# Performance work log

Hardware: AMD Instinct MI355X
Metric: run time of the kernel (lower is better)

## Reference

```python
import jax, jax.numpy as jnp
import numpy as np

B, N, C, H, NH, NC = 4, 2048, 256, 128, 8, 3  # batch, points, in_ch, hidden, heads, classes
DH = H // NH


def setup_inputs() -> dict:
    key = jax.random.key(0)
    ki = iter(jax.random.split(key, 48))
    def w(shape, s=0.05):
        return jax.random.normal(next(ki), shape, jnp.float32) * s
    z = lambda n: jnp.zeros((n,), jnp.float32)
    o = lambda n: jnp.ones((n,), jnp.float32)
    inp = dict(x=jax.random.normal(next(ki), (B, N, C), jnp.float32))
    inp.update(fuse_w1=w((H, C)), fuse_b1=z(H), fuse_w2=w((H, H)), fuse_b2=z(H))
    for l in range(2):
        inp[f'attn{l}_in_w'] = w((3 * H, H)); inp[f'attn{l}_in_b'] = z(3 * H)
        inp[f'attn{l}_out_w'] = w((H, H)); inp[f'attn{l}_out_b'] = z(H)
        inp[f'ffn{l}_w1'] = w((2 * H, H)); inp[f'ffn{l}_b1'] = z(2 * H)
        inp[f'ffn{l}_w2'] = w((H, 2 * H)); inp[f'ffn{l}_b2'] = z(H)
        inp[f'ln{2*l}_g'] = o(H); inp[f'ln{2*l}_b'] = z(H)
        inp[f'ln{2*l+1}_g'] = o(H); inp[f'ln{2*l+1}_b'] = z(H)
    inp.update(out_w1=w((H, H)), out_b1=z(H), out_w2=w((NC, H)), out_b2=z(NC))
    inp.update(det_w1=w((H // 2, H)), det_b1=z(H // 2), det_w2=w((1, H // 2)), det_b2=z(1))
    return inp


def _ln(x, g, b):
    m = jnp.mean(x, axis=-1, keepdims=True)
    v = jnp.mean((x - m) ** 2, axis=-1, keepdims=True)
    return (x - m) * jax.lax.rsqrt(v + 1e-5) * g + b


def _mha(x, in_w, in_b, out_w, out_b):
    # nn.MultiheadAttention (batch_first, self-attn), eval mode (no dropout)
    Bq, Nq, _ = x.shape
    qkv = x @ in_w.T + in_b                          # [B,N,3H]
    q, k, v = jnp.split(qkv, 3, axis=-1)
    q = q.reshape(Bq, Nq, NH, DH)
    k = k.reshape(Bq, Nq, NH, DH)
    v = v.reshape(Bq, Nq, NH, DH)
    s = jnp.einsum('bqhd,bkhd->bhqk', q, k) / jnp.sqrt(jnp.float32(DH))
    a = jax.nn.softmax(s, axis=-1)
    o = jnp.einsum('bhqk,bkhd->bqhd', a, v).reshape(Bq, Nq, H)
    return o @ out_w.T + out_b


def _forward(x, fuse_w1, fuse_b1, fuse_w2, fuse_b2,
             attn0_in_w, attn0_in_b, attn0_out_w, attn0_out_b,
             ffn0_w1, ffn0_b1, ffn0_w2, ffn0_b2, ln0_g, ln0_b, ln1_g, ln1_b,
             attn1_in_w, attn1_in_b, attn1_out_w, attn1_out_b,
             ffn1_w1, ffn1_b1, ffn1_w2, ffn1_b2, ln2_g, ln2_b, ln3_g, ln3_b,
             out_w1, out_b1, out_w2, out_b2, det_w1, det_b1, det_w2, det_b2):
    # feature_fusion (dropout = identity in eval)
    h = jnp.maximum(x @ fuse_w1.T + fuse_b1, 0) @ fuse_w2.T + fuse_b2
    layers = [
        (attn0_in_w, attn0_in_b, attn0_out_w, attn0_out_b, ffn0_w1, ffn0_b1, ffn0_w2, ffn0_b2, ln0_g, ln0_b, ln1_g, ln1_b),
        (attn1_in_w, attn1_in_b, attn1_out_w, attn1_out_b, ffn1_w1, ffn1_b1, ffn1_w2, ffn1_b2, ln2_g, ln2_b, ln3_g, ln3_b),
    ]
    for (iw, ib, ow, ob, f1w, f1b, f2w, f2b, g1, be1, g2, be2) in layers:
        h = _ln(h + _mha(h, iw, ib, ow, ob), g1, be1)
        h = _ln(h + (jnp.maximum(h @ f1w.T + f1b, 0) @ f2w.T + f2b), g2, be2)
    refined_logits = jnp.maximum(h @ out_w1.T + out_b1, 0) @ out_w2.T + out_b2   # [B,N,NC]
    head_prob = jax.nn.sigmoid(jnp.maximum(h @ det_w1.T + det_b1, 0) @ det_w2.T + det_b2)[..., 0]  # [B,N]
    quality = jnp.mean(head_prob, axis=1)                                        # [B]
    return refined_logits, head_prob, quality


def reference(x, fuse_w1, fuse_b1, fuse_w2, fuse_b2,
              attn0_in_w, attn0_in_b, attn0_out_w, attn0_out_b,
              ffn0_w1, ffn0_b1, ffn0_w2, ffn0_b2, ln0_g, ln0_b, ln1_g, ln1_b,
              attn1_in_w, attn1_in_b, attn1_out_w, attn1_out_b,
              ffn1_w1, ffn1_b1, ffn1_w2, ffn1_b2, ln2_g, ln2_b, ln3_g, ln3_b,
              out_w1, out_b1, out_w2, out_b2, det_w1, det_b1, det_w2, det_b2):
    return _forward(x, fuse_w1, fuse_b1, fuse_w2, fuse_b2,
                    attn0_in_w, attn0_in_b, attn0_out_w, attn0_out_b,
                    ffn0_w1, ffn0_b1, ffn0_w2, ffn0_b2, ln0_g, ln0_b, ln1_g, ln1_b,
                    attn1_in_w, attn1_in_b, attn1_out_w, attn1_out_b,
                    ffn1_w1, ffn1_b1, ffn1_w2, ffn1_b2, ln2_g, ln2_b, ln3_g, ln3_b,
                    out_w1, out_b1, out_w2, out_b2, det_w1, det_b1, det_w2, det_b2)
```

## Files before the change

kernel.cpp:

```cpp
#include <hip/hip_runtime.h>
#include <cstddef>

constexpr int Bb  = 4;
constexpr int Nn  = 2048;
constexpr int Cc  = 256;
constexpr int Hh  = 128;
constexpr int NHh = 8;
constexpr int DHh = 16;
constexpr int MTOK = Bb * Nn;
#define LOG2E 1.4426950408889634f

typedef __attribute__((ext_vector_type(8))) short bf16x8;
typedef __attribute__((ext_vector_type(4))) short bf16x4;
typedef __attribute__((ext_vector_type(4))) float f32x4;

__device__ __forceinline__ short f32_to_bf16_rne(float f) {
    union { float f; unsigned int u; } c; c.f = f;
    unsigned int r = c.u + 0x7fffu + ((c.u >> 16) & 1u);
    return (short)(r >> 16);
}
__device__ __forceinline__ float bf16_to_f32(short s) {
    union { float f; unsigned int u; } c; c.u = ((unsigned int)(unsigned short)s) << 16;
    return c.f;
}
__device__ __forceinline__ unsigned pack2_bf16(float a, float b) {
    unsigned ua = __float_as_uint(a);
    unsigned ub = __float_as_uint(b);
    ua += 0x7fffu + ((ua >> 16) & 1u);
    ub += 0x7fffu + ((ub >> 16) & 1u);
    return __builtin_amdgcn_perm(ub, ua, 0x07060302);
}

struct CvtJobs {
    const float* src[13];
    short*       dst[13];
    int          off[14];
    float*       qzero;
};

__global__ __launch_bounds__(256) void cvt_kernel(CvtJobs j) {
    const int gid = blockIdx.x * 256 + threadIdx.x;
    if (blockIdx.x == 0 && threadIdx.x < 4) j.qzero[threadIdx.x] = 0.f;
    if (gid >= j.off[13]) return;
    int k = 0;
    #pragma unroll
    for (int i = 0; i < 12; ++i) if (gid >= j.off[i + 1]) k = i + 1;
    const int idx = (gid - j.off[k]) * 4;
    float4 v = *(const float4*)(j.src[k] + idx);
    short o4[4] = { f32_to_bf16_rne(v.x), f32_to_bf16_rne(v.y),
                    f32_to_bf16_rne(v.z), f32_to_bf16_rne(v.w) };
    *(bf16x4*)(j.dst[k] + idx) = *(bf16x4*)o4;
}

__global__ __launch_bounds__(256) void gemm_qkv_kernel(
    const short* __restrict__ X, const short* __restrict__ W,
    const float* __restrict__ bias, short* __restrict__ Yb)
{
    constexpr int K = 128, N = 384;
    __shared__ short As[64 * 40];
    __shared__ short Bs[64 * 40];

    const int tid  = threadIdx.x;
    const int lane = tid & 63;
    const int wv   = tid >> 6;
    const int col  = lane & 15;
    const int g    = lane >> 4;
    const int m0   = blockIdx.y * 64;
    const int n0   = blockIdx.x * 64;
    const int sr   = tid >> 2;
    const int sc   = (tid & 3) * 8;

    f32x4 acc[4] = {};

    for (int k0 = 0; k0 < K; k0 += 32) {
        __syncthreads();
        *(bf16x8*)&As[sr * 40 + sc] =
            *(const bf16x8*)(X + (size_t)(m0 + sr) * K + k0 + sc);
        *(bf16x8*)&Bs[sr * 40 + sc] =
            *(const bf16x8*)(W + (size_t)(n0 + sr) * K + k0 + sc);
        __syncthreads();

        bf16x8 a = *(bf16x8*)&As[(wv * 16 + col) * 40 + g * 8];
        #pragma unroll
        for (int jj = 0; jj < 4; ++jj) {
            bf16x8 b = *(bf16x8*)&Bs[(jj * 16 + col) * 40 + g * 8];
            acc[jj] = __builtin_amdgcn_mfma_f32_16x16x32_bf16(a, b, acc[jj], 0, 0, 0);
        }
    }

    #pragma unroll
    for (int jj = 0; jj < 4; ++jj) {
        const int cn  = n0 + jj * 16 + col;
        const int sec = cn >> 7;
        const int hd  = (cn & 127) >> 4;
        const int d   = cn & 15;
        const float bb = bias[cn];
        #pragma unroll
        for (int r = 0; r < 4; ++r) {
            const int rm = m0 + wv * 16 + g * 4 + r;
            const int bq = rm >> 11, tt = rm & 2047;
            float v = acc[jj][r] + bb;
            Yb[(size_t)sec * (MTOK * 128)
               + ((size_t)(bq * NHh + hd) * Nn + tt) * DHh + d] = f32_to_bf16_rne(v);
        }
    }
}

template<int K, int CR, bool DO_LN>
__global__ __launch_bounds__(256) void gemmln_kernel(
    const short* __restrict__ X, const short* __restrict__ W,
    const float* __restrict__ bias,
    float* __restrict__ hf, short* __restrict__ hb,
    const float* __restrict__ gw, const float* __restrict__ bw)
{
    constexpr int ST  = K + 8;
    constexpr int NCH = 128 / CR;
    constexpr int NF  = CR / 32;
    __shared__ short As[32 * ST];
    __shared__ short Ws[CR * ST];
    __shared__ float P[32 * 130];

    const int tid  = threadIdx.x;
    const int lane = tid & 63;
    const int wv   = tid >> 6;
    const int col  = lane & 15;
    const int g    = lane >> 4;
    const int m0   = blockIdx.x * 32;
    const int mst  = (wv & 1) * 16;
    const int cb   = (wv >> 1) * (CR / 2);

    for (int i = tid; i < 32 * (K / 8); i += 256) {
        const int r = i / (K / 8), c = (i % (K / 8)) * 8;
        *(bf16x8*)&As[r * ST + c] = *(const bf16x8*)(X + (size_t)(m0 + r) * K + c);
    }

    f32x4 ya[NCH][NF] = {};
    #pragma unroll
    for (int ch = 0; ch < NCH; ++ch) {
        for (int i = tid; i < CR * (K / 8); i += 256) {
            const int r = i / (K / 8), c = (i % (K / 8)) * 8;
            *(bf16x8*)&Ws[r * ST + c] =
                *(const bf16x8*)(W + (size_t)(ch * CR + r) * K + c);
        }
        __syncthreads();
        #pragma unroll
        for (int k0 = 0; k0 < K; k0 += 32) {
            bf16x8 a = *(bf16x8*)&As[(mst + col) * ST + k0 + g * 8];
            #pragma unroll
            for (int f = 0; f < NF; ++f) {
                bf16x8 b = *(bf16x8*)&Ws[(cb + f * 16 + col) * ST + k0 + g * 8];
                ya[ch][f] = __builtin_amdgcn_mfma_f32_16x16x32_bf16(a, b, ya[ch][f], 0, 0, 0);
            }
        }
        __syncthreads();
    }

    #pragma unroll
    for (int ch = 0; ch < NCH; ++ch)
        #pragma unroll
        for (int f = 0; f < NF; ++f) {
            const int cn = ch * CR + cb + f * 16 + col;
            const float bb = bias[cn];
            #pragma unroll
            for (int r = 0; r < 4; ++r)
                P[(mst + g * 4 + r) * 130 + cn] = ya[ch][f][r] + bb;
        }
    __syncthreads();

    #pragma unroll
    for (int rr = 0; rr < 8; ++rr) {
        const int row = wv * 8 + rr;
        const size_t t = m0 + row;
        float2 pv = *(float2*)&P[row * 130 + 2 * lane];
        if (DO_LN) {
            float2 hv = ((const float2*)(hf + t * Hh))[lane];
            float a0 = hv.x + pv.x, a1 = hv.y + pv.y;
            float sum = a0 + a1;
            #pragma unroll
            for (int off = 32; off > 0; off >>= 1) sum += __shfl_xor(sum, off);
            const float mean = sum * (1.f / 128.f);
            const float d0 = a0 - mean, d1 = a1 - mean;
            float vs = d0 * d0 + d1 * d1;
            #pragma unroll
            for (int off = 32; off > 0; off >>= 1) vs += __shfl_xor(vs, off);
            const float rstd = rsqrtf(vs * (1.f / 128.f) + 1e-5f);
            float2 gv = ((const float2*)gw)[lane];
            float2 bv = ((const float2*)bw)[lane];
            float2 r = { d0 * rstd * gv.x + bv.x, d1 * rstd * gv.y + bv.y };
            ((float2*)(hf + t * Hh))[lane] = r;
            *(unsigned*)&hb[t * Hh + lane * 2] = pack2_bf16(r.x, r.y);
        } else {
            ((float2*)(hf + t * Hh))[lane] = pv;
            *(unsigned*)&hb[t * Hh + lane * 2] = pack2_bf16(pv.x, pv.y);
        }
    }
}

template<int K, int MID, int CR1, int CR2, bool DO_LN>
__global__ __launch_bounds__(256) void mlp2_kernel(
    const short* __restrict__ X,
    const short* __restrict__ W1, const float* __restrict__ b1,
    const short* __restrict__ W2, const float* __restrict__ b2,
    float* __restrict__ hf, short* __restrict__ hb,
    const float* __restrict__ gw, const float* __restrict__ bw)
{
    constexpr int STA = K + 8;
    constexpr int STU = MID + 8;
    constexpr int WS1 = CR1 * STA;
    constexpr int WS2 = CR2 * STU;
    constexpr int WSZ = (WS1 > WS2) ? WS1 : WS2;
    __shared__ short As[32 * STA];
    __shared__ short Ws[WSZ];
    __shared__ short U[32 * STU];
    __shared__ float P[32 * 130];

    const int tid  = threadIdx.x;
    const int lane = tid & 63;
    const int wv   = tid >> 6;
    const int col  = lane & 15;
    const int g    = lane >> 4;
    const int m0   = blockIdx.x * 32;
    const int mst  = (wv & 1) * 16;

    for (int i = tid; i < 32 * (K / 8); i += 256) {
        const int r = i / (K / 8), c = (i % (K / 8)) * 8;
        *(bf16x8*)&As[r * STA + c] = *(const bf16x8*)(X + (size_t)(m0 + r) * K + c);
    }

    constexpr int NCH1 = MID / CR1;
    constexpr int NF1  = CR1 / 32;
    const int cb1 = (wv >> 1) * (CR1 / 2);
    #pragma unroll
    for (int ch = 0; ch < NCH1; ++ch) {
        for (int i = tid; i < CR1 * (K / 8); i += 256) {
            const int r = i / (K / 8), c = (i % (K / 8)) * 8;
            *(bf16x8*)&Ws[r * STA + c] =
                *(const bf16x8*)(W1 + (size_t)(ch * CR1 + r) * K + c);
        }
        __syncthreads();
        f32x4 ya[NF1] = {};
        #pragma unroll
        for (int k0 = 0; k0 < K; k0 += 32) {
            bf16x8 a = *(bf16x8*)&As[(mst + col) * STA + k0 + g * 8];
            #pragma unroll
            for (int f = 0; f < NF1; ++f) {
                bf16x8 b = *(bf16x8*)&Ws[(cb1 + f * 16 + col) * STA + k0 + g * 8];
                ya[f] = __builtin_amdgcn_mfma_f32_16x16x32_bf16(a, b, ya[f], 0, 0, 0);
            }
        }
        #pragma unroll
        for (int f = 0; f < NF1; ++f) {
            const int cn = ch * CR1 + cb1 + f * 16 + col;
            const float bb = b1[cn];
            #pragma unroll
            for (int r = 0; r < 4; ++r)
                U[(mst + g * 4 + r) * STU + cn] =
                    f32_to_bf16_rne(fmaxf(ya[f][r] + bb, 0.f));
        }
        __syncthreads();
    }

    constexpr int NCH2 = 128 / CR2;
    constexpr int NF2  = CR2 / 32;
    const int cb2 = (wv >> 1) * (CR2 / 2);
    f32x4 yb[NCH2][NF2] = {};
    #pragma unroll
    for (int ch = 0; ch < NCH2; ++ch) {
        for (int i = tid; i < CR2 * (MID / 8); i += 256) {
            const int r = i / (MID / 8), c = (i % (MID / 8)) * 8;
            *(bf16x8*)&Ws[r * STU + c] =
                *(const bf16x8*)(W2 + (size_t)(ch * CR2 + r) * MID + c);
        }
        __syncthreads();
        #pragma unroll
        for (int k0 = 0; k0 < MID; k0 += 32) {
            bf16x8 a = *(bf16x8*)&U[(mst + col) * STU + k0 + g * 8];
            #pragma unroll
            for (int f = 0; f < NF2; ++f) {
                bf16x8 b = *(bf16x8*)&Ws[(cb2 + f * 16 + col) * STU + k0 + g * 8];
                yb[ch][f] = __builtin_amdgcn_mfma_f32_16x16x32_bf16(a, b, yb[ch][f], 0, 0, 0);
            }
        }
        __syncthreads();
    }

    #pragma unroll
    for (int ch = 0; ch < NCH2; ++ch)
        #pragma unroll
        for (int f = 0; f < NF2; ++f) {
            const int cn = ch * CR2 + cb2 + f * 16 + col;
            const float bb = b2[cn];
            #pragma unroll
            for (int r = 0; r < 4; ++r)
                P[(mst + g * 4 + r) * 130 + cn] = yb[ch][f][r] + bb;
        }
    __syncthreads();

    #pragma unroll
    for (int rr = 0; rr < 8; ++rr) {
        const int row = wv * 8 + rr;
        const size_t t = m0 + row;
        float2 pv = *(float2*)&P[row * 130 + 2 * lane];
        if (DO_LN) {
            float2 hv = ((const float2*)(hf + t * Hh))[lane];
            float a0 = hv.x + pv.x, a1 = hv.y + pv.y;
            float sum = a0 + a1;
            #pragma unroll
            for (int off = 32; off > 0; off >>= 1) sum += __shfl_xor(sum, off);
            const float mean = sum * (1.f / 128.f);
            const float d0 = a0 - mean, d1 = a1 - mean;
            float vs = d0 * d0 + d1 * d1;
            #pragma unroll
            for (int off = 32; off > 0; off >>= 1) vs += __shfl_xor(vs, off);
            const float rstd = rsqrtf(vs * (1.f / 128.f) + 1e-5f);
            float2 gv = ((const float2*)gw)[lane];
            float2 bv = ((const float2*)bw)[lane];
            float2 r = { d0 * rstd * gv.x + bv.x, d1 * rstd * gv.y + bv.y };
            ((float2*)(hf + t * Hh))[lane] = r;
            *(unsigned*)&hb[t * Hh + lane * 2] = pack2_bf16(r.x, r.y);
        } else {
            ((float2*)(hf + t * Hh))[lane] = pv;
            *(unsigned*)&hb[t * Hh + lane * 2] = pack2_bf16(pv.x, pv.y);
        }
    }
}

__global__ __launch_bounds__(256) void head_kernel(
    const short* __restrict__ X,
    const short* __restrict__ W1b, const float* __restrict__ b1,
    const short* __restrict__ DW1b, const float* __restrict__ db1,
    const float* __restrict__ w2, const float* __restrict__ b2,
    const float* __restrict__ dw2, const float* __restrict__ db2,
    float* __restrict__ out)
{
    constexpr int K = 128, ST = K + 8;
    __shared__ short As[32 * ST];
    __shared__ short Ws[64 * ST];
    __shared__ float P[32 * 196];

    const int tid  = threadIdx.x;
    const int lane = tid & 63;
    const int wv   = tid >> 6;
    const int col  = lane & 15;
    const int g    = lane >> 4;
    const int m0   = blockIdx.x * 32;
    const int mst  = (wv & 1) * 16;
    const int cb   = (wv >> 1) * 32;

    for (int i = tid; i < 32 * (K / 8); i += 256) {
        const int r = i / (K / 8), c = (i % (K / 8)) * 8;
        *(bf16x8*)&As[r * ST + c] = *(const bf16x8*)(X + (size_t)(m0 + r) * K + c);
    }

    f32x4 ya[3][2] = {};
    #pragma unroll
    for (int ch = 0; ch < 3; ++ch) {
        for (int i = tid; i < 64 * (K / 8); i += 256) {
            const int r = i / (K / 8), c = (i % (K / 8)) * 8;
            const int rg = ch * 64 + r;
            const short* src = (rg < 128) ? (W1b + (size_t)rg * K)
                                          : (DW1b + (size_t)(rg - 128) * K);
            *(bf16x8*)&Ws[r * ST + c] = *(const bf16x8*)(src + c);
        }
        __syncthreads();
        #pragma unroll
        for (int k0 = 0; k0 < K; k0 += 32) {
            bf16x8 a = *(bf16x8*)&As[(mst + col) * ST + k0 + g * 8];
            #pragma unroll
            for (int f = 0; f < 2; ++f) {
                bf16x8 b = *(bf16x8*)&Ws[(cb + f * 16 + col) * ST + k0 + g * 8];
                ya[ch][f] = __builtin_amdgcn_mfma_f32_16x16x32_bf16(a, b, ya[ch][f], 0, 0, 0);
            }
        }
        __syncthreads();
    }

    #pragma unroll
    for (int ch = 0; ch < 3; ++ch)
        #pragma unroll
        for (int f = 0; f < 2; ++f) {
            const int cn = ch * 64 + cb + f * 16 + col;
            const float bb = (cn < 128) ? b1[cn] : db1[cn - 128];
            #pragma unroll
            for (int r = 0; r < 4; ++r)
                P[(mst + g * 4 + r) * 196 + cn] = fmaxf(ya[ch][f][r] + bb, 0.f);
        }
    __syncthreads();

    const float w20 = w2[2 * lane],       w21 = w2[2 * lane + 1];
    const float w22 = w2[128 + 2 * lane], w23 = w2[129 + 2 * lane];
    const float w24 = w2[256 + 2 * lane], w25 = w2[257 + 2 * lane];
    const float dwl = dw2[lane];
    float qacc = 0.f;
    #pragma unroll
    for (int rr = 0; rr < 8; ++rr) {
        const int row = wv * 8 + rr;
        const size_t t = m0 + row;
        const float x0 = P[row * 196 + 2 * lane];
        const float x1 = P[row * 196 + 2 * lane + 1];
        float s0 = x0 * w20 + x1 * w21;
        float s1 = x0 * w22 + x1 * w23;
        float s2 = x0 * w24 + x1 * w25;
        float d  = P[row * 196 + 128 + lane] * dwl;
        #pragma unroll
        for (int off = 32; off > 0; off >>= 1) {
            s0 += __shfl_xor(s0, off);
            s1 += __shfl_xor(s1, off);
            s2 += __shfl_xor(s2, off);
            d  += __shfl_xor(d,  off);
        }
        if (lane == 0) {
            out[t * 3 + 0] = s0 + b2[0];
            out[t * 3 + 1] = s1 + b2[1];
            out[t * 3 + 2] = s2 + b2[2];
            const float prob = 1.f / (1.f + __expf(-(d + db2[0])));
            out[24576 + t] = prob;
            qacc += prob;
        }
    }
    if (lane == 0)
        atomicAdd(&out[32768 + (m0 >> 11)], qacc * (1.f / (float)Nn));
}

constexpr int KT = 128;
constexpr int KS = 28;
constexpr int VS = 132;

__global__ __launch_bounds__(256) void attn_kernel(
    const short* __restrict__ qkv, short* __restrict__ out)
{
    __shared__ short Ks[KT * KS];
    __shared__ short Vs[DHh * VS];

    const int tid  = threadIdx.x;
    const int lane = tid & 63;
    const int wv   = tid >> 6;
    const int col  = lane & 15;
    const int g    = lane >> 4;
    const int hd   = blockIdx.y;
    const int b    = blockIdx.z;
    const int q0   = blockIdx.x * 64 + wv * 16;

    const size_t bh = (size_t)(b * NHh + hd) * Nn * DHh;
    const short* Qh = qkv + bh;
    const short* Kh = qkv + (size_t)MTOK * 128 + bh;
    const short* Vh = qkv + (size_t)2 * MTOK * 128 + bh;

    bf16x8 qf = {};
    if (g < 2) {
        bf16x8 qraw = *(const bf16x8*)(Qh + (size_t)(q0 + col) * DHh + g * 8);
        const float qs = 0.25f * LOG2E;
        #pragma unroll
        for (int i = 0; i < 8; ++i)
            qf[i] = f32_to_bf16_rne(bf16_to_f32(qraw[i]) * qs);
    }

    f32x4 o    = {0.f, 0.f, 0.f, 0.f};
    f32x4 lacc = {0.f, 0.f, 0.f, 0.f};
    const short one_bf16 = (short)0x3F80;
    const bf16x8 ones = { one_bf16, one_bf16, one_bf16, one_bf16,
                          one_bf16, one_bf16, one_bf16, one_bf16 };

    const int ksr = tid >> 1;
    const int ksd = (tid & 1) * 8;
    const int va  = tid >> 2;
    const int vd  = (tid & 3) * 4;

    for (int kt = 0; kt < Nn; kt += KT) {
        __syncthreads();
        {
            *(bf16x8*)&Ks[ksr * KS + ksd] =
                *(const bf16x8*)(Kh + (size_t)(kt + ksr) * DHh + ksd);
            const short* v0 = Vh + (size_t)(kt + 2 * va) * DHh + vd;
            bf16x4 r0 = *(const bf16x4*)v0;
            bf16x4 r1 = *(const bf16x4*)(v0 + DHh);
            unsigned a0 = ((const unsigned*)&r0)[0], a1 = ((const unsigned*)&r0)[1];
            unsigned b0 = ((const unsigned*)&r1)[0], b1 = ((const unsigned*)&r1)[1];
            *(unsigned*)&Vs[(vd + 0) * VS + 2 * va] = __builtin_amdgcn_perm(b0, a0, 0x05040100);
            *(unsigned*)&Vs[(vd + 1) * VS + 2 * va] = __builtin_amdgcn_perm(b0, a0, 0x07060302);
            *(unsigned*)&Vs[(vd + 2) * VS + 2 * va] = __builtin_amdgcn_perm(b1, a1, 0x05040100);
            *(unsigned*)&Vs[(vd + 3) * VS + 2 * va] = __builtin_amdgcn_perm(b1, a1, 0x07060302);
        }
        __syncthreads();

        #pragma unroll
        for (int s = 0; s < 4; ++s) {
            bf16x8 kf0 = {}, kf1 = {};
            if (g < 2) {
                kf0 = *(bf16x8*)&Ks[(s * 32 + col) * KS + g * 8];
                kf1 = *(bf16x8*)&Ks[(s * 32 + 16 + col) * KS + g * 8];
            }
            f32x4 z = {0.f, 0.f, 0.f, 0.f};
            f32x4 sA = __builtin_amdgcn_mfma_f32_16x16x32_bf16(kf0, qf, z, 0, 0, 0);
            f32x4 sB = __builtin_amdgcn_mfma_f32_16x16x32_bf16(kf1, qf, z, 0, 0, 0);

            union { bf16x8 v; unsigned u[4]; } pf;
            pf.u[0] = pack2_bf16(__builtin_amdgcn_exp2f(sA[0]),
                                 __builtin_amdgcn_exp2f(sA[1]));
            pf.u[1] = pack2_bf16(__builtin_amdgcn_exp2f(sA[2]),
                                 __builtin_amdgcn_exp2f(sA[3]));
            pf.u[2] = pack2_bf16(__builtin_amdgcn_exp2f(sB[0]),
                                 __builtin_amdgcn_exp2f(sB[1]));
            pf.u[3] = pack2_bf16(__builtin_amdgcn_exp2f(sB[2]),
                                 __builtin_amdgcn_exp2f(sB[3]));

            bf16x8 vf;
            ((bf16x4*)&vf)[0] = *(bf16x4*)&Vs[col * VS + s * 32 + g * 4];
            ((bf16x4*)&vf)[1] = *(bf16x4*)&Vs[col * VS + s * 32 + 16 + g * 4];

            o    = __builtin_amdgcn_mfma_f32_16x16x32_bf16(pf.v, vf,   o,    0, 0, 0);
            lacc = __builtin_amdgcn_mfma_f32_16x16x32_bf16(pf.v, ones, lacc, 0, 0, 0);
        }
    }

    #pragma unroll
    for (int r = 0; r < 4; ++r) {
        const float inv = __builtin_amdgcn_rcpf(lacc[r]);
        out[(size_t)(b * Nn + q0 + g * 4 + r) * Hh + hd * DHh + col] =
            f32_to_bf16_rne(o[r] * inv);
    }
}

extern "C" void kernel_launch(void* const* d_in, const int* in_sizes, int n_in,
                              void* d_out, int out_size, void* d_ws, size_t ws_size,
                              hipStream_t stream)
{
    char* W8 = (char*)d_ws;
    float* hf   = (float*)(W8 + 0);
    short* hb   = (short*)(W8 + 4194304);
    short* wb   = (short*)(W8 + 6291456);
    char*  regA = W8 + 7340032;
    char*  regB = W8 + 13631488;

    short* xb    = (short*)regA;
    short* qkvb  = (short*)regA;
    short* attno = (short*)regB;
    float* out   = (float*)d_out;

    const int wsz[12]  = {32768,16384,49152,16384,32768,32768,49152,16384,32768,32768,16384,8192};
    const int wsrc[12] = {1, 3, 5, 7, 9, 11, 17, 19, 21, 23, 29, 33};
    int woff[13]; woff[0] = 0;
    for (int i = 0; i < 12; ++i) woff[i + 1] = woff[i] + wsz[i];

    CvtJobs jobs;
    int acc = 0;
    for (int i = 0; i < 12; ++i) {
        jobs.src[i] = (const float*)d_in[wsrc[i]];
        jobs.dst[i] = wb + woff[i];
        jobs.off[i] = acc;
        acc += wsz[i] / 4;
    }
    jobs.src[12] = (const float*)d_in[0];
    jobs.dst[12] = xb;
    jobs.off[12] = acc;
    acc += (MTOK * Cc) / 4;
    jobs.off[13] = acc;
    jobs.qzero = out + 32768;

    hipLaunchKernelGGL(cvt_kernel, dim3((acc + 255) / 256), dim3(256), 0, stream, jobs);

    hipLaunchKernelGGL((mlp2_kernel<256, 128, 32, 64, false>), dim3(MTOK / 32), dim3(256), 0,
                       stream, xb, wb + woff[0], (const float*)d_in[2],
                       wb + woff[1], (const float*)d_in[4], hf, hb, nullptr, nullptr);

    for (int l = 0; l < 2; ++l) {
        const int ib = 5 + l * 12;
        const int wbase = 2 + l * 4;
        hipLaunchKernelGGL(gemm_qkv_kernel, dim3(384 / 64, MTOK / 64), dim3(256), 0, stream,
                           hb, wb + woff[wbase + 0], (const float*)d_in[ib + 1], qkvb);
        hipLaunchKernelGGL(attn_kernel, dim3(Nn / 64, NHh, Bb), dim3(256), 0, stream,
                           qkvb, attno);
        hipLaunchKernelGGL((gemmln_kernel<128, 64, true>), dim3(MTOK / 32), dim3(256), 0, stream,
                           attno, wb + woff[wbase + 1], (const float*)d_in[ib + 3],
                           hf, hb, (const float*)d_in[ib + 8], (const float*)d_in[ib + 9]);
        hipLaunchKernelGGL((mlp2_kernel<128, 256, 64, 32, true>), dim3(MTOK / 32), dim3(256), 0,
                           stream, hb, wb + woff[wbase + 2], (const float*)d_in[ib + 5],
                           wb + woff[wbase + 3], (const float*)d_in[ib + 7],
                           hf, hb, (const float*)d_in[ib + 10], (const float*)d_in[ib + 11]);
    }

    hipLaunchKernelGGL(head_kernel, dim3(MTOK / 32), dim3(256), 0, stream,
                       hb, wb + woff[10], (const float*)d_in[30],
                       wb + woff[11], (const float*)d_in[34],
                       (const float*)d_in[31], (const float*)d_in[32],
                       (const float*)d_in[35], (const float*)d_in[36], out);
}
```

Baseline: 299.9 us.

## Fuse out-proj, LN, FFN and next-layer QKV into per-layer kernels

Result: slower. 306.7 us (+2.3%).

```diff
diff --git a/kernel.cpp b/kernel.cpp
--- a/kernel.cpp
+++ b/kernel.cpp
@@ -52,72 +52,34 @@
     *(bf16x4*)(j.dst[k] + idx) = *(bf16x4*)o4;
 }
 
-__global__ __launch_bounds__(256) void gemm_qkv_kernel(
-    const short* __restrict__ X, const short* __restrict__ W,
-    const float* __restrict__ bias, short* __restrict__ Yb)
+__device__ __forceinline__ void stage_w(short* Ws, const short* src, int rows,
+                                        int kw, int st, int tid) {
+    for (int i = tid; i < rows * (kw / 8); i += 256) {
+        const int r = i / (kw / 8), c = (i % (kw / 8)) * 8;
+        *(bf16x8*)&Ws[r * st + c] = *(const bf16x8*)(src + (size_t)r * kw + c);
+    }
+}
+
+__device__ __forceinline__ void qkv_write(short* qkvb, int rm, int cn, float v) {
+    const int sec = cn >> 7;
+    const int hd  = (cn & 127) >> 4;
+    const int d   = cn & 15;
+    const int bq  = rm >> 11, tt = rm & 2047;
+    qkvb[(size_t)sec * (MTOK * 128)
+         + ((size_t)(bq * NHh + hd) * Nn + tt) * DHh + d] = f32_to_bf16_rne(v);
+}
+
+__global__ __launch_bounds__(256) void fusion_qkv_kernel(
+    const short* __restrict__ X,
+    const short* __restrict__ W1, const float* __restrict__ b1,
+    const short* __restrict__ W2, const float* __restrict__ b2,
+    float* __restrict__ hf, short* __restrict__ hb,
+    const short* __restrict__ Wq, const float* __restrict__ bq,
+    short* __restrict__ qkvb)
 {
-    constexpr int K = 128, N = 384;
-    __shared__ short As[64 * 40];
-    __shared__ short Bs[64 * 40];
-
-    const int tid  = threadIdx.x;
-    const int lane = tid & 63;
-    const int wv   = tid >> 6;
-    const int col  = lane & 15;
-    const int g    = lane >> 4;
-    const int m0   = blockIdx.y * 64;
-    const int n0   = blockIdx.x * 64;
-    const int sr   = tid >> 2;
-    const int sc   = (tid & 3) * 8;
-
-    f32x4 acc[4] = {};
-
-    for (int k0 = 0; k0 < K; k0 += 32) {
-        __syncthreads();
-        *(bf16x8*)&As[sr * 40 + sc] =
-            *(const bf16x8*)(X + (size_t)(m0 + sr) * K + k0 + sc);
-        *(bf16x8*)&Bs[sr * 40 + sc] =
-            *(const bf16x8*)(W + (size_t)(n0 + sr) * K + k0 + sc);
-        __syncthreads();
-
-        bf16x8 a = *(bf16x8*)&As[(wv * 16 + col) * 40 + g * 8];
-        #pragma unroll
-        for (int jj = 0; jj < 4; ++jj) {
-            bf16x8 b = *(bf16x8*)&Bs[(jj * 16 + col) * 40 + g * 8];
-            acc[jj] = __builtin_amdgcn_mfma_f32_16x16x32_bf16(a, b, acc[jj], 0, 0, 0);
-        }
-    }
-
-    #pragma unroll
-    for (int jj = 0; jj < 4; ++jj) {
-        const int cn  = n0 + jj * 16 + col;
-        const int sec = cn >> 7;
-        const int hd  = (cn & 127) >> 4;
-        const int d   = cn & 15;
-        const float bb = bias[cn];
-        #pragma unroll
-        for (int r = 0; r < 4; ++r) {
-            const int rm = m0 + wv * 16 + g * 4 + r;
-            const int bq = rm >> 11, tt = rm & 2047;
-            float v = acc[jj][r] + bb;
-            Yb[(size_t)sec * (MTOK * 128)
-               + ((size_t)(bq * NHh + hd) * Nn + tt) * DHh + d] = f32_to_bf16_rne(v);
-        }
-    }
-}
-
-template<int K, int CR, bool DO_LN>
-__global__ __launch_bounds__(256) void gemmln_kernel(
-    const short* __restrict__ X, const short* __restrict__ W,
-    const float* __restrict__ bias,
-    float* __restrict__ hf, short* __restrict__ hb,
-    const float* __restrict__ gw, const float* __restrict__ bw)
-{
-    constexpr int ST  = K + 8;
-    constexpr int NCH = 128 / CR;
-    constexpr int NF  = CR / 32;
-    __shared__ short As[32 * ST];
-    __shared__ short Ws[CR * ST];
+    __shared__ short As[32 * 264];
+    __shared__ short Ws[8704];
+    __shared__ short U[32 * 136];
     __shared__ float P[32 * 130];
 
     const int tid  = threadIdx.x;
@@ -127,91 +89,121 @@
     const int g    = lane >> 4;
     const int m0   = blockIdx.x * 32;
     const int mst  = (wv & 1) * 16;
-    const int cb   = (wv >> 1) * (CR / 2);
-
-    for (int i = tid; i < 32 * (K / 8); i += 256) {
-        const int r = i / (K / 8), c = (i % (K / 8)) * 8;
-        *(bf16x8*)&As[r * ST + c] = *(const bf16x8*)(X + (size_t)(m0 + r) * K + c);
-    }
-
-    f32x4 ya[NCH][NF] = {};
-    #pragma unroll
-    for (int ch = 0; ch < NCH; ++ch) {
-        for (int i = tid; i < CR * (K / 8); i += 256) {
-            const int r = i / (K / 8), c = (i % (K / 8)) * 8;
-            *(bf16x8*)&Ws[r * ST + c] =
-                *(const bf16x8*)(W + (size_t)(ch * CR + r) * K + c);
-        }
+
+    for (int i = tid; i < 32 * (256 / 8); i += 256) {
+        const int r = i / 32, c = (i % 32) * 8;
+        *(bf16x8*)&As[r * 264 + c] = *(const bf16x8*)(X + (size_t)(m0 + r) * 256 + c);
+    }
+
+    {
+        const int cb1 = (wv >> 1) * 16;
+        #pragma unroll
+        for (int ch = 0; ch < 4; ++ch) {
+            stage_w(Ws, W1 + (size_t)(ch * 32) * 256, 32, 256, 264, tid);
+            __syncthreads();
+            f32x4 ya = {0.f, 0.f, 0.f, 0.f};
+            #pragma unroll
+            for (int k0 = 0; k0 < 256; k0 += 32) {
+                bf16x8 a = *(bf16x8*)&As[(mst + col) * 264 + k0 + g * 8];
+                bf16x8 b = *(bf16x8*)&Ws[(cb1 + col) * 264 + k0 + g * 8];
+                ya = __builtin_amdgcn_mfma_f32_16x16x32_bf16(a, b, ya, 0, 0, 0);
+            }
+            const int cn = ch * 32 + cb1 + col;
+            const float bb = b1[cn];
+            #pragma unroll
+            for (int r = 0; r < 4; ++r)
+                U[(mst + g * 4 + r) * 136 + cn] =
+                    f32_to_bf16_rne(fmaxf(ya[r] + bb, 0.f));
+            __syncthreads();
+        }
+    }
+
+    {
+        const int cb2 = (wv >> 1) * 32;
+        f32x4 yb[2][2] = {};
+        #pragma unroll
+        for (int ch = 0; ch < 2; ++ch) {
+            stage_w(Ws, W2 + (size_t)(ch * 64) * 128, 64, 128, 136, tid);
+            __syncthreads();
+            #pragma unroll
+            for (int k0 = 0; k0 < 128; k0 += 32) {
+                bf16x8 a = *(bf16x8*)&U[(mst + col) * 136 + k0 + g * 8];
+                #pragma unroll
+                for (int f = 0; f < 2; ++f) {
+                    bf16x8 b = *(bf16x8*)&Ws[(cb2 + f * 16 + col) * 136 + k0 + g * 8];
+                    yb[ch][f] = __builtin_amdgcn_mfma_f32_16x16x32_bf16(a, b, yb[ch][f], 0, 0, 0);
+                }
+            }
+            __syncthreads();
+        }
+        #pragma unroll
+        for (int ch = 0; ch < 2; ++ch)
+            #pragma unroll
+            for (int f = 0; f < 2; ++f) {
+                const int cn = ch * 64 + cb2 + f * 16 + col;
+                const float bb = b2[cn];
+                #pragma unroll
+                for (int r = 0; r < 4; ++r)
+                    P[(mst + g * 4 + r) * 130 + cn] = yb[ch][f][r] + bb;
+            }
         __syncthreads();
-        #pragma unroll
-        for (int k0 = 0; k0 < K; k0 += 32) {
-            bf16x8 a = *(bf16x8*)&As[(mst + col) * ST + k0 + g * 8];
-            #pragma unroll
-            for (int f = 0; f < NF; ++f) {
-                bf16x8 b = *(bf16x8*)&Ws[(cb + f * 16 + col) * ST + k0 + g * 8];
-                ya[ch][f] = __builtin_amdgcn_mfma_f32_16x16x32_bf16(a, b, ya[ch][f], 0, 0, 0);
-            }
-        }
-        __syncthreads();
-    }
-
-    #pragma unroll
-    for (int ch = 0; ch < NCH; ++ch)
-        #pragma unroll
-        for (int f = 0; f < NF; ++f) {
-            const int cn = ch * CR + cb + f * 16 + col;
-            const float bb = bias[cn];
-            #pragma unroll
-            for (int r = 0; r < 4; ++r)
-                P[(mst + g * 4 + r) * 130 + cn] = ya[ch][f][r] + bb;
-        }
-    __syncthreads();
+    }
 
     #pragma unroll
     for (int rr = 0; rr < 8; ++rr) {
         const int row = wv * 8 + rr;
         const size_t t = m0 + row;
         float2 pv = *(float2*)&P[row * 130 + 2 * lane];
-        if (DO_LN) {
-            float2 hv = ((const float2*)(hf + t * Hh))[lane];
-            float a0 = hv.x + pv.x, a1 = hv.y + pv.y;
-            float sum = a0 + a1;
-            #pragma unroll
-            for (int off = 32; off > 0; off >>= 1) sum += __shfl_xor(sum, off);
-            const float mean = sum * (1.f / 128.f);
-            const float d0 = a0 - mean, d1 = a1 - mean;
-            float vs = d0 * d0 + d1 * d1;
-            #pragma unroll
-            for (int off = 32; off > 0; off >>= 1) vs += __shfl_xor(vs, off);
-            const float rstd = rsqrtf(vs * (1.f / 128.f) + 1e-5f);
-            float2 gv = ((const float2*)gw)[lane];
-            float2 bv = ((const float2*)bw)[lane];
-            float2 r = { d0 * rstd * gv.x + bv.x, d1 * rstd * gv.y + bv.y };
-            ((float2*)(hf + t * Hh))[lane] = r;
-            *(unsigned*)&hb[t * Hh + lane * 2] = pack2_bf16(r.x, r.y);
-        } else {
-            ((float2*)(hf + t * Hh))[lane] = pv;
-            *(unsigned*)&hb[t * Hh + lane * 2] = pack2_bf16(pv.x, pv.y);
-        }
-    }
-}
-
-template<int K, int MID, int CR1, int CR2, bool DO_LN>
-__global__ __launch_bounds__(256) void mlp2_kernel(
+        ((float2*)(hf + t * Hh))[lane] = pv;
+        const unsigned pk = pack2_bf16(pv.x, pv.y);
+        *(unsigned*)&hb[t * Hh + lane * 2] = pk;
+        *(unsigned*)&U[row * 136 + 2 * lane] = pk;
+    }
+
+    {
+        const int cb = (wv >> 1) * 32;
+        #pragma unroll
+        for (int ch = 0; ch < 6; ++ch) {
+            stage_w(Ws, Wq + (size_t)(ch * 64) * 128, 64, 128, 136, tid);
+            __syncthreads();
+            f32x4 yq[2] = {};
+            #pragma unroll
+            for (int k0 = 0; k0 < 128; k0 += 32) {
+                bf16x8 a = *(bf16x8*)&U[(mst + col) * 136 + k0 + g * 8];
+                #pragma unroll
+                for (int f = 0; f < 2; ++f) {
+                    bf16x8 b = *(bf16x8*)&Ws[(cb + f * 16 + col) * 136 + k0 + g * 8];
+                    yq[f] = __builtin_amdgcn_mfma_f32_16x16x32_bf16(a, b, yq[f], 0, 0, 0);
+                }
+            }
+            #pragma unroll
+            for (int f = 0; f < 2; ++f) {
+                const int cn = ch * 64 + cb + f * 16 + col;
+                const float bb = bq[cn];
+                #pragma unroll
+                for (int r = 0; r < 4; ++r)
+                    qkv_write(qkvb, m0 + mst + g * 4 + r, cn, yq[f][r] + bb);
+            }
+            __syncthreads();
+        }
+    }
+}
+
+template<bool DO_QKV>
+__global__ __launch_bounds__(256) void layer_kernel(
     const short* __restrict__ X,
+    const short* __restrict__ Wo, const float* __restrict__ bo,
+    const float* __restrict__ g1v, const float* __restrict__ be1v,
     const short* __restrict__ W1, const float* __restrict__ b1,
     const short* __restrict__ W2, const float* __restrict__ b2,
+    const float* __restrict__ g2v, const float* __restrict__ be2v,
     float* __restrict__ hf, short* __restrict__ hb,
-    const float* __restrict__ gw, const float* __restrict__ bw)
+    const short* __restrict__ Wq, const float* __restrict__ bq,
+    short* __restrict__ qkvb)
 {
-    constexpr int STA = K + 8;
-    constexpr int STU = MID + 8;
-    constexpr int WS1 = CR1 * STA;
-    constexpr int WS2 = CR2 * STU;
-    constexpr int WSZ = (WS1 > WS2) ? WS1 : WS2;
-    __shared__ short As[32 * STA];
-    __shared__ short Ws[WSZ];
-    __shared__ short U[32 * STU];
+    __shared__ short As[32 * 136];
+    __shared__ short Ws[8704];
+    __shared__ short U[32 * 264];
     __shared__ float P[32 * 130];
 
     const int tid  = threadIdx.x;
@@ -222,105 +214,171 @@
     const int m0   = blockIdx.x * 32;
     const int mst  = (wv & 1) * 16;
 
-    for (int i = tid; i < 32 * (K / 8); i += 256) {
-        const int r = i / (K / 8), c = (i % (K / 8)) * 8;
-        *(bf16x8*)&As[r * STA + c] = *(const bf16x8*)(X + (size_t)(m0 + r) * K + c);
-    }
-
-    constexpr int NCH1 = MID / CR1;
-    constexpr int NF1  = CR1 / 32;
-    const int cb1 = (wv >> 1) * (CR1 / 2);
-    #pragma unroll
-    for (int ch = 0; ch < NCH1; ++ch) {
-        for (int i = tid; i < CR1 * (K / 8); i += 256) {
-            const int r = i / (K / 8), c = (i % (K / 8)) * 8;
-            *(bf16x8*)&Ws[r * STA + c] =
-                *(const bf16x8*)(W1 + (size_t)(ch * CR1 + r) * K + c);
-        }
+    for (int i = tid; i < 32 * (128 / 8); i += 256) {
+        const int r = i / 16, c = (i % 16) * 8;
+        *(bf16x8*)&As[r * 136 + c] = *(const bf16x8*)(X + (size_t)(m0 + r) * 128 + c);
+    }
+
+    {
+        const int cb = (wv >> 1) * 32;
+        f32x4 yo[2][2] = {};
+        #pragma unroll
+        for (int ch = 0; ch < 2; ++ch) {
+            stage_w(Ws, Wo + (size_t)(ch * 64) * 128, 64, 128, 136, tid);
+            __syncthreads();
+            #pragma unroll
+            for (int k0 = 0; k0 < 128; k0 += 32) {
+                bf16x8 a = *(bf16x8*)&As[(mst + col) * 136 + k0 + g * 8];
+                #pragma unroll
+                for (int f = 0; f < 2; ++f) {
+                    bf16x8 b = *(bf16x8*)&Ws[(cb + f * 16 + col) * 136 + k0 + g * 8];
+                    yo[ch][f] = __builtin_amdgcn_mfma_f32_16x16x32_bf16(a, b, yo[ch][f], 0, 0, 0);
+                }
+            }
+            __syncthreads();
+        }
+        #pragma unroll
+        for (int ch = 0; ch < 2; ++ch)
+            #pragma unroll
+            for (int f = 0; f < 2; ++f) {
+                const int cn = ch * 64 + cb + f * 16 + col;
+                const float bb = bo[cn];
+                #pragma unroll
+                for (int r = 0; r < 4; ++r)
+                    P[(mst + g * 4 + r) * 130 + cn] = yo[ch][f][r] + bb;
+            }
         __syncthreads();
-        f32x4 ya[NF1] = {};
-        #pragma unroll
-        for (int k0 = 0; k0 < K; k0 += 32) {
-            bf16x8 a = *(bf16x8*)&As[(mst + col) * STA + k0 + g * 8];
-            #pragma unroll
-            for (int f = 0; f < NF1; ++f) {
-                bf16x8 b = *(bf16x8*)&Ws[(cb1 + f * 16 + col) * STA + k0 + g * 8];
-                ya[f] = __builtin_amdgcn_mfma_f32_16x16x32_bf16(a, b, ya[f], 0, 0, 0);
-            }
-        }
-        #pragma unroll
-        for (int f = 0; f < NF1; ++f) {
-            const int cn = ch * CR1 + cb1 + f * 16 + col;
-            const float bb = b1[cn];
-            #pragma unroll
-            for (int r = 0; r < 4; ++r)
-                U[(mst + g * 4 + r) * STU + cn] =
-                    f32_to_bf16_rne(fmaxf(ya[f][r] + bb, 0.f));
-        }
-        __syncthreads();
-    }
-
-    constexpr int NCH2 = 128 / CR2;
-    constexpr int NF2  = CR2 / 32;
-    const int cb2 = (wv >> 1) * (CR2 / 2);
-    f32x4 yb[NCH2][NF2] = {};
-    #pragma unroll
-    for (int ch = 0; ch < NCH2; ++ch) {
-        for (int i = tid; i < CR2 * (MID / 8); i += 256) {
-            const int r = i / (MID / 8), c = (i % (MID / 8)) * 8;
-            *(bf16x8*)&Ws[r * STU + c] =
-                *(const bf16x8*)(W2 + (size_t)(ch * CR2 + r) * MID + c);
-        }
-        __syncthreads();
-        #pragma unroll
-        for (int k0 = 0; k0 < MID; k0 += 32) {
-            bf16x8 a = *(bf16x8*)&U[(mst + col) * STU + k0 + g * 8];
-            #pragma unroll
-            for (int f = 0; f < NF2; ++f) {
-                bf16x8 b = *(bf16x8*)&Ws[(cb2 + f * 16 + col) * STU + k0 + g * 8];
-                yb[ch][f] = __builtin_amdgcn_mfma_f32_16x16x32_bf16(a, b, yb[ch][f], 0, 0, 0);
-            }
-        }
-        __syncthreads();
-    }
-
-    #pragma unroll
-    for (int ch = 0; ch < NCH2; ++ch)
-        #pragma unroll
-        for (int f = 0; f < NF2; ++f) {
-            const int cn = ch * CR2 + cb2 + f * 16 + col;
-            const float bb = b2[cn];
-            #pragma unroll
-            for (int r = 0; r < 4; ++r)
-                P[(mst + g * 4 + r) * 130 + cn] = yb[ch][f][r] + bb;
-        }
-    __syncthreads();
-
+    }
+
+    float2 res[8];
     #pragma unroll
     for (int rr = 0; rr < 8; ++rr) {
         const int row = wv * 8 + rr;
         const size_t t = m0 + row;
         float2 pv = *(float2*)&P[row * 130 + 2 * lane];
-        if (DO_LN) {
-            float2 hv = ((const float2*)(hf + t * Hh))[lane];
-            float a0 = hv.x + pv.x, a1 = hv.y + pv.y;
-            float sum = a0 + a1;
-            #pragma unroll
-            for (int off = 32; off > 0; off >>= 1) sum += __shfl_xor(sum, off);
-            const float mean = sum * (1.f / 128.f);
-            const float d0 = a0 - mean, d1 = a1 - mean;
-            float vs = d0 * d0 + d1 * d1;
-            #pragma unroll
-            for (int off = 32; off > 0; off >>= 1) vs += __shfl_xor(vs, off);
-            const float rstd = rsqrtf(vs * (1.f / 128.f) + 1e-5f);
-            float2 gv = ((const float2*)gw)[lane];
-            float2 bv = ((const float2*)bw)[lane];
-            float2 r = { d0 * rstd * gv.x + bv.x, d1 * rstd * gv.y + bv.y };
-            ((float2*)(hf + t * Hh))[lane] = r;
-            *(unsigned*)&hb[t * Hh + lane * 2] = pack2_bf16(r.x, r.y);
-        } else {
-            ((float2*)(hf + t * Hh))[lane] = pv;
-            *(unsigned*)&hb[t * Hh + lane * 2] = pack2_bf16(pv.x, pv.y);
+        float2 hv = ((const float2*)(hf + t * Hh))[lane];
+        float a0 = hv.x + pv.x, a1 = hv.y + pv.y;
+        float sum = a0 + a1;
+        #pragma unroll
+        for (int off = 32; off > 0; off >>= 1) sum += __shfl_xor(sum, off);
+        const float mean = sum * (1.f / 128.f);
+        const float d0 = a0 - mean, d1 = a1 - mean;
+        float vs = d0 * d0 + d1 * d1;
+        #pragma unroll
+        for (int off = 32; off > 0; off >>= 1) vs += __shfl_xor(vs, off);
+        const float rstd = rsqrtf(vs * (1.f / 128.f) + 1e-5f);
+        float2 gv = ((const float2*)g1v)[lane];
+        float2 bv = ((const float2*)be1v)[lane];
+        float2 r = { d0 * rstd * gv.x + bv.x, d1 * rstd * gv.y + bv.y };
+        res[rr] = r;
+        *(unsigned*)&As[row * 136 + 2 * lane] = pack2_bf16(r.x, r.y);
+    }
+
+    {
+        const int cb1 = (wv >> 1) * 32;
+        #pragma unroll
+        for (int ch = 0; ch < 4; ++ch) {
+            stage_w(Ws, W1 + (size_t)(ch * 64) * 128, 64, 128, 136, tid);
+            __syncthreads();
+            f32x4 ya[2] = {};
+            #pragma unroll
+            for (int k0 = 0; k0 < 128; k0 += 32) {
+                bf16x8 a = *(bf16x8*)&As[(mst + col) * 136 + k0 + g * 8];
+                #pragma unroll
+                for (int f = 0; f < 2; ++f) {
+                    bf16x8 b = *(bf16x8*)&Ws[(cb1 + f * 16 + col) * 136 + k0 + g * 8];
+                    ya[f] = __builtin_amdgcn_mfma_f32_16x16x32_bf16(a, b, ya[f], 0, 0, 0);
+                }
+            }
+            #pragma unroll
+            for (int f = 0; f < 2; ++f) {
+                const int cn = ch * 64 + cb1 + f * 16 + col;
+                const float bb = b1[cn];
+                #pragma unroll
+                for (int r = 0; r < 4; ++r)
+                    U[(mst + g * 4 + r) * 264 + cn] =
+                        f32_to_bf16_rne(fmaxf(ya[f][r] + bb, 0.f));
+            }
+            __syncthreads();
+        }
+    }
+
+    {
+        const int cb2 = (wv >> 1) * 16;
+        f32x4 yf2[4] = {};
+        #pragma unroll
+        for (int ch = 0; ch < 4; ++ch) {
+            stage_w(Ws, W2 + (size_t)(ch * 32) * 256, 32, 256, 264, tid);
+            __syncthreads();
+            #pragma unroll
+            for (int k0 = 0; k0 < 256; k0 += 32) {
+                bf16x8 a = *(bf16x8*)&U[(mst + col) * 264 + k0 + g * 8];
+                bf16x8 b = *(bf16x8*)&Ws[(cb2 + col) * 264 + k0 + g * 8];
+                yf2[ch] = __builtin_amdgcn_mfma_f32_16x16x32_bf16(a, b, yf2[ch], 0, 0, 0);
+            }
+            __syncthreads();
+        }
+        #pragma unroll
+        for (int ch = 0; ch < 4; ++ch) {
+            const int cn = ch * 32 + cb2 + col;
+            const float bb = b2[cn];
+            #pragma unroll
+            for (int r = 0; r < 4; ++r)
+                P[(mst + g * 4 + r) * 130 + cn] = yf2[ch][r] + bb;
+        }
+        __syncthreads();
+    }
+
+    #pragma unroll
+    for (int rr = 0; rr < 8; ++rr) {
+        const int row = wv * 8 + rr;
+        const size_t t = m0 + row;
+        float2 pv = *(float2*)&P[row * 130 + 2 * lane];
+        float a0 = res[rr].x + pv.x, a1 = res[rr].y + pv.y;
+        float sum = a0 + a1;
+        #pragma unroll
+        for (int off = 32; off > 0; off >>= 1) sum += __shfl_xor(sum, off);
+        const float mean = sum * (1.f / 128.f);
+        const float d0 = a0 - mean, d1 = a1 - mean;
+        float vs = d0 * d0 + d1 * d1;
+        #pragma unroll
+        for (int off = 32; off > 0; off >>= 1) vs += __shfl_xor(vs, off);
+        const float rstd = rsqrtf(vs * (1.f / 128.f) + 1e-5f);
+        float2 gv = ((const float2*)g2v)[lane];
+        float2 bv = ((const float2*)be2v)[lane];
+        float2 r = { d0 * rstd * gv.x + bv.x, d1 * rstd * gv.y + bv.y };
+        ((float2*)(hf + t * Hh))[lane] = r;
+        const unsigned pk = pack2_bf16(r.x, r.y);
+        *(unsigned*)&hb[t * Hh + lane * 2] = pk;
+        if (DO_QKV)
+            *(unsigned*)&As[row * 136 + 2 * lane] = pk;
+    }
+
+    if (DO_QKV) {
+        const int cb = (wv >> 1) * 32;
+        #pragma unroll
+        for (int ch = 0; ch < 6; ++ch) {
+            stage_w(Ws, Wq + (size_t)(ch * 64) * 128, 64, 128, 136, tid);
+            __syncthreads();
+            f32x4 yq[2] = {};
+            #pragma unroll
+            for (int k0 = 0; k0 < 128; k0 += 32) {
+                bf16x8 a = *(bf16x8*)&As[(mst + col) * 136 + k0 + g * 8];
+                #pragma unroll
+                for (int f = 0; f < 2; ++f) {
+                    bf16x8 b = *(bf16x8*)&Ws[(cb + f * 16 + col) * 136 + k0 + g * 8];
+                    yq[f] = __builtin_amdgcn_mfma_f32_16x16x32_bf16(a, b, yq[f], 0, 0, 0);
+                }
+            }
+            #pragma unroll
+            for (int f = 0; f < 2; ++f) {
+                const int cn = ch * 64 + cb + f * 16 + col;
+                const float bb = bq[cn];
+                #pragma unroll
+                for (int r = 0; r < 4; ++r)
+                    qkv_write(qkvb, m0 + mst + g * 4 + r, cn, yq[f][r] + bb);
+            }
+            __syncthreads();
         }
     }
 }
@@ -526,15 +584,12 @@
                               hipStream_t stream)
 {
     char* W8 = (char*)d_ws;
-    float* hf   = (float*)(W8 + 0);
-    short* hb   = (short*)(W8 + 4194304);
-    short* wb   = (short*)(W8 + 6291456);
-    char*  regA = W8 + 7340032;
-    char*  regB = W8 + 13631488;
-
-    short* xb    = (short*)regA;
-    short* qkvb  = (short*)regA;
-    short* attno = (short*)regB;
+    float* hf    = (float*)(W8 + 0);
+    short* hb    = (short*)(W8 + 4194304);
+    short* wb    = (short*)(W8 + 6291456);
+    short* xb    = (short*)(W8 + 7340032);
+    short* attno = (short*)(W8 + 13631488);
+    short* qkvb  = (short*)(W8 + 16777216);
     float* out   = (float*)d_out;
 
     const int wsz[12]  = {32768,16384,49152,16384,32768,32768,49152,16384,32768,32768,16384,8192};
@@ -559,25 +614,32 @@
 
     hipLaunchKernelGGL(cvt_kernel, dim3((acc + 255) / 256), dim3(256), 0, stream, jobs);
 
-    hipLaunchKernelGGL((mlp2_kernel<256, 128, 32, 64, false>), dim3(MTOK / 32), dim3(256), 0,
-                       stream, xb, wb + woff[0], (const float*)d_in[2],
-                       wb + woff[1], (const float*)d_in[4], hf, hb, nullptr, nullptr);
-
-    for (int l = 0; l < 2; ++l) {
-        const int ib = 5 + l * 12;
-        const int wbase = 2 + l * 4;
-        hipLaunchKernelGGL(gemm_qkv_kernel, dim3(384 / 64, MTOK / 64), dim3(256), 0, stream,
-                           hb, wb + woff[wbase + 0], (const float*)d_in[ib + 1], qkvb);
-        hipLaunchKernelGGL(attn_kernel, dim3(Nn / 64, NHh, Bb), dim3(256), 0, stream,
-                           qkvb, attno);
-        hipLaunchKernelGGL((gemmln_kernel<128, 64, true>), dim3(MTOK / 32), dim3(256), 0, stream,
-                           attno, wb + woff[wbase + 1], (const float*)d_in[ib + 3],
-                           hf, hb, (const float*)d_in[ib + 8], (const float*)d_in[ib + 9]);
-        hipLaunchKernelGGL((mlp2_kernel<128, 256, 64, 32, true>), dim3(MTOK / 32), dim3(256), 0,
-                           stream, hb, wb + woff[wbase + 2], (const float*)d_in[ib + 5],
-                           wb + woff[wbase + 3], (const float*)d_in[ib + 7],
-                           hf, hb, (const float*)d_in[ib + 10], (const float*)d_in[ib + 11]);
-    }
+    hipLaunchKernelGGL(fusion_qkv_kernel, dim3(MTOK / 32), dim3(256), 0, stream,
+                       xb, wb + woff[0], (const float*)d_in[2],
+                       wb + woff[1], (const float*)d_in[4], hf, hb,
+                       wb + woff[2], (const float*)d_in[6], qkvb);
+
+    hipLaunchKernelGGL(attn_kernel, dim3(Nn / 64, NHh, Bb), dim3(256), 0, stream,
+                       qkvb, attno);
+
+    hipLaunchKernelGGL((layer_kernel<true>), dim3(MTOK / 32), dim3(256), 0, stream,
+                       attno, wb + woff[3], (const float*)d_in[8],
+                       (const float*)d_in[13], (const float*)d_in[14],
+                       wb + woff[4], (const float*)d_in[10],
+                       wb + woff[5], (const float*)d_in[12],
+                       (const float*)d_in[15], (const float*)d_in[16],
+                       hf, hb, wb + woff[6], (const float*)d_in[18], qkvb);
+
+    hipLaunchKernelGGL(attn_kernel, dim3(Nn / 64, NHh, Bb), dim3(256), 0, stream,
+                       qkvb, attno);
+
+    hipLaunchKernelGGL((layer_kernel<false>), dim3(MTOK / 32), dim3(256), 0, stream,
+                       attno, wb + woff[7], (const float*)d_in[20],
+                       (const float*)d_in[25], (const float*)d_in[26],
+                       wb + woff[8], (const float*)d_in[22],
+                       wb + woff[9], (const float*)d_in[24],
+                       (const float*)d_in[27], (const float*)d_in[28],
+                       hf, hb, nullptr, nullptr, nullptr);
 
     hipLaunchKernelGGL(head_kernel, dim3(MTOK / 32), dim3(256), 0, stream,
                        hb, wb + woff[10], (const float*)d_in[30],
```
